# Kernel tuning notes

Hardware: AMD Instinct MI355X
Metric: run time of the kernel (lower is better)

Reference implementation:

```python
import jax, jax.numpy as jnp
import numpy as np

B, T, C, L = 512, 512, 96, 64   # batch, time steps, num classes (incl. blank), max label len
BLANK = C - 1                   # keras ctc_batch_cost uses last class as blank
EPS = 1e-7                      # epsilon added before log, as in ctc_batch_cost
NEG = -1e30                     # log-space -inf surrogate


def setup_inputs():
    key = jax.random.key(0)
    k1, k2, k3 = jax.random.split(key, 3)
    # y_pred is a softmax output: positive, rows sum to 1
    u = jax.random.uniform(k1, (B, T, C), dtype=jnp.float32, minval=0.1, maxval=1.0)
    y_pred = u / jnp.sum(u, axis=-1, keepdims=True)
    # labels in [0, BLANK), variable lengths, padded with -1 (as the layer expects)
    labels = jax.random.randint(k2, (B, L), 0, C - 1, dtype=jnp.int32)
    lens = jax.random.randint(k3, (B,), L // 2, L + 1, dtype=jnp.int32)
    y_true = jnp.where(jnp.arange(L)[None, :] < lens[:, None], labels, -1)
    return {"y_true": y_true, "y_pred": y_pred}


def _ctc_loss(y_true, y_pred):
    """Per-example CTC negative log-likelihood (forward DP in log space)."""
    y_true = y_true.astype(jnp.int32)
    lbl_len = jnp.sum((y_true != -1).astype(jnp.int32), axis=-1)          # (B,)
    labels = jnp.where(y_true != -1, y_true, 0)                            # (B,L)

    S = 2 * L + 1
    # extended label: blank, l0, blank, l1, ..., blank
    ext = jnp.full((B, S), BLANK, dtype=jnp.int32).at[:, 1::2].set(labels)  # (B,S)
    ext_m2 = jnp.pad(ext[:, :-2], ((0, 0), (2, 0)), constant_values=BLANK)
    can_skip = (ext != BLANK) & (ext != ext_m2)                             # (B,S)

    lp = jnp.log(y_pred.astype(jnp.float32) + EPS)   # (B,T,C) log-probs
    lp_t = jnp.swapaxes(lp, 0, 1)                    # (T,B,C) for scan over time

    emit0 = jnp.take_along_axis(lp_t[0], ext, axis=1)                       # (B,S)
    alpha0 = (jnp.full((B, S), NEG, dtype=jnp.float32)
              .at[:, 0].set(emit0[:, 0])
              .at[:, 1].set(emit0[:, 1]))

    def step(alpha, lpt):
        a1 = jnp.pad(alpha[:, :-1], ((0, 0), (1, 0)), constant_values=NEG)
        a2 = jnp.pad(alpha[:, :-2], ((0, 0), (2, 0)), constant_values=NEG)
        a2 = jnp.where(can_skip, a2, NEG)
        m = jnp.maximum(alpha, jnp.maximum(a1, a2))
        lse = m + jnp.log(jnp.exp(alpha - m) + jnp.exp(a1 - m) + jnp.exp(a2 - m))
        alpha_new = lse + jnp.take_along_axis(lpt, ext, axis=1)
        return alpha_new, None

    alphaT, _ = jax.lax.scan(step, alpha0, lp_t[1:])

    # total log-prob ends at last blank (s=2*len) or last label (s=2*len-1)
    i_blank = (2 * lbl_len)[:, None]
    i_label = jnp.maximum(2 * lbl_len - 1, 0)[:, None]
    a_b = jnp.take_along_axis(alphaT, i_blank, axis=1)[:, 0]
    a_l = jnp.take_along_axis(alphaT, i_label, axis=1)[:, 0]
    return -jnp.logaddexp(a_b, a_l)                                         # (B,)


def reference(y_true, y_pred):
    # layer adds tf.reduce_mean(ctc_batch_cost(...)) as the model loss
    return jnp.mean(_ctc_loss(y_true, y_pred))
```

## Files before the change

### kernel.cpp

```cpp
#include <hip/hip_runtime.h>


#define B_ 512
#define T_ 512
#define C_ 96
#define L_ 64
#define BLANK_ 95
#define EPSF 1e-7f
#define LN2F 0.69314718055994530942f

template <int CTRL>
__device__ __forceinline__ float dpp_mov(float x) {
    return __int_as_float(
        __builtin_amdgcn_update_dpp(0, __float_as_int(x), CTRL, 0xF, 0xF, true));
}

__device__ __forceinline__ float wave_max(float m) {
    m = fmaxf(m, dpp_mov<0x111>(m));
    m = fmaxf(m, dpp_mov<0x112>(m));
    m = fmaxf(m, dpp_mov<0x114>(m));
    m = fmaxf(m, dpp_mov<0x118>(m));
    m = fmaxf(m, dpp_mov<0x142>(m));
    m = fmaxf(m, dpp_mov<0x143>(m));
    return __int_as_float(__builtin_amdgcn_readlane(__float_as_int(m), 63));
}

__launch_bounds__(64, 1)
__global__ void ctc_loss_kernel(const int* __restrict__ y_true,
                                const float* __restrict__ y_pred,
                                float* __restrict__ out) {
    const int b = blockIdx.x;
    const int lane = threadIdx.x;

    const int yv = y_true[b * L_ + lane];
    const unsigned long long act = __ballot(yv != -1);
    const int len = __popcll(act);
    const int lab = (yv == -1) ? 0 : yv;
    const int lab_prev = __shfl_up(lab, 1);
    const bool cs = (lane == 0) ? true : (lab != lab_prev);

    const float* rowp = y_pred + (size_t)b * T_ * C_;
    const float* plp = rowp + lab;
    const float* pbp = rowp + BLANK_;

    constexpr int U = 8;
    constexpr int D = 8;
    constexpr int NCH = T_ / U;
    float bl[D][U], bb[D][U];
#pragma unroll
    for (int d = 0; d < D; ++d)
#pragma unroll
        for (int k = 0; k < U; ++k) {
            bl[d][k] = plp[(d * U + k) * C_];
            bb[d][k] = pbp[(d * U + k) * C_];
        }

    float a_even, a_odd, a128;
    int accum = -96;
    a_even = (lane == 0) ? ldexpf(bb[0][0] + EPSF, 96) : 0.0f;
    a_odd  = (lane == 0) ? ldexpf(bl[0][0] + EPSF, 96) : 0.0f;
    a128 = 0.0f;

    auto chunk_exec = [&](const float* cl, const float* cb, int kstart) {
        float pl[U], pb[U], mpl[U];
#pragma unroll
        for (int k = 0; k < U; ++k) {
            pl[k] = cl[k] + EPSF;
            pb[k] = cb[k] + EPSF;
            mpl[k] = cs ? pl[k] : 0.0f;
        }
#pragma unroll
        for (int k = 0; k < U; ++k) {
            if (k < kstart) continue;
            const float po = dpp_mov<0x138>(a_odd);
            const float ne = fmaf(po, pb[k], a_even * pb[k]);
            const float no = fmaf(po, mpl[k], (a_odd + a_even) * pl[k]);
            a128 = fmaf(a_odd, pb[k], a128 * pb[k]);
            a_even = ne;
            a_odd = no;
        }
        const float mv = wave_max(fmaxf(fmaxf(a_even, a_odd), a128));
        const int e = ((__float_as_int(mv) >> 23) & 0xFF) - 126;
        const int kk = 96 - e;
        a_even = ldexpf(a_even, kk);
        a_odd  = ldexpf(a_odd, kk);
        a128   = ldexpf(a128, kk);
        accum -= kk;
    };

    auto prefetch = [&](float* dl, float* db, int t0) {
#pragma unroll
        for (int k = 0; k < U; ++k) {
            dl[k] = plp[(t0 + k) * C_];
            db[k] = pbp[(t0 + k) * C_];
        }
    };

#pragma unroll
    for (int sub = 0; sub < D; ++sub) {
        chunk_exec(bl[sub], bb[sub], (sub == 0) ? 1 : 0);
        prefetch(bl[sub], bb[sub], (sub + D) * U);
    }

    for (int g = 1; g < NCH / D; ++g) {
#pragma unroll
        for (int sub = 0; sub < D; ++sub) {
            const int c = g * D + sub;
            chunk_exec(bl[sub], bb[sub], 0);
            if (c + D < NCH) prefetch(bl[sub], bb[sub], (c + D) * U);
        }
    }

    const float al = __shfl(a_odd, len - 1);
    const float ab = (len < L_) ? __shfl(a_even, len)
                                : __shfl(a128, 63);
    if (lane == 0) {
        const float loss = -LN2F * (log2f(ab + al) + (float)accum);
        atomicAdd(out, loss * (1.0f / B_));
    }
}

extern "C" void kernel_launch(void* const* d_in, const int* in_sizes, int n_in,
                              void* d_out, int out_size, void* d_ws, size_t ws_size,
                              hipStream_t stream) {
    const int* y_true = (const int*)d_in[0];
    const float* y_pred = (const float*)d_in[1];
    float* out = (float*)d_out;
    hipMemsetAsync(out, 0, sizeof(float), stream);
    ctc_loss_kernel<<<B_, 64, 0, stream>>>(y_true, y_pred, out);
}
```

Measured before the change: 156.9 us.

## Stage y_pred chunks through double-buffered LDS with coalesced float4 loads

Each lane used to do scalar strided gathers from global memory for its label column and the blank column at every timestep. Now whole 8-timestep chunks are loaded with coalesced float4 reads into a register ring four chunks deep. They are copied into a double-buffered LDS slot and gathered from there. The t=0 initialisation is folded into the recurrence by seeding lane 0's even state with 2^96, so the first step needs no special case. This cuts global load instruction count and uncoalesced traffic, but puts LDS round-trip latency and extra writes onto the serial DP chain.

After: 192.1 us. 1.22x slower.

```diff
diff --git a/kernel.cpp b/kernel.cpp
--- a/kernel.cpp
+++ b/kernel.cpp
@@ -39,75 +39,78 @@
     const int lab_prev = __shfl_up(lab, 1);
     const bool cs = (lane == 0) ? true : (lab != lab_prev);
 
-    const float* rowp = y_pred + (size_t)b * T_ * C_;
-    const float* plp = rowp + lab;
-    const float* pbp = rowp + BLANK_;
+    constexpr int U = 8;
+    constexpr int D = 4;
+    constexpr int NCH = T_ / U;
+    constexpr int CHW = U * C_;
 
-    constexpr int U = 8;
-    constexpr int D = 8;
-    constexpr int NCH = T_ / U;
-    float bl[D][U], bb[D][U];
+    const float* __restrict__ gbase = y_pred + (size_t)b * T_ * C_ + lane * 4;
+
+    __shared__ __align__(16) float smem[2 * CHW];
+
+    float4 ring[D][3];
 #pragma unroll
     for (int d = 0; d < D; ++d)
 #pragma unroll
-        for (int k = 0; k < U; ++k) {
-            bl[d][k] = plp[(d * U + k) * C_];
-            bb[d][k] = pbp[(d * U + k) * C_];
-        }
+        for (int j = 0; j < 3; ++j)
+            ring[d][j] = *reinterpret_cast<const float4*>(gbase + d * CHW + j * 256);
+#pragma unroll
+    for (int j = 0; j < 3; ++j)
+        *reinterpret_cast<float4*>(&smem[(j * 64 + lane) * 4]) = ring[0][j];
 
-    float a_even, a_odd, a128;
+    float a_even = (lane == 0) ? 0x1.0p96f : 0.0f;
+    float a_odd = 0.0f;
+    float a128 = 0.0f;
     int accum = -96;
-    a_even = (lane == 0) ? ldexpf(bb[0][0] + EPSF, 96) : 0.0f;
-    a_odd  = (lane == 0) ? ldexpf(bl[0][0] + EPSF, 96) : 0.0f;
-    a128 = 0.0f;
 
-    auto chunk_exec = [&](const float* cl, const float* cb, int kstart) {
-        float pl[U], pb[U], mpl[U];
+    for (int cc = 0; cc < NCH; cc += D) {
 #pragma unroll
-        for (int k = 0; k < U; ++k) {
-            pl[k] = cl[k] + EPSF;
-            pb[k] = cb[k] + EPSF;
-            mpl[k] = cs ? pl[k] : 0.0f;
-        }
+        for (int sub = 0; sub < D; ++sub) {
+            const int c = cc + sub;
+
+            if (c + D < NCH) {
 #pragma unroll
-        for (int k = 0; k < U; ++k) {
-            if (k < kstart) continue;
-            const float po = dpp_mov<0x138>(a_odd);
-            const float ne = fmaf(po, pb[k], a_even * pb[k]);
-            const float no = fmaf(po, mpl[k], (a_odd + a_even) * pl[k]);
-            a128 = fmaf(a_odd, pb[k], a128 * pb[k]);
-            a_even = ne;
-            a_odd = no;
-        }
-        const float mv = wave_max(fmaxf(fmaxf(a_even, a_odd), a128));
-        const int e = ((__float_as_int(mv) >> 23) & 0xFF) - 126;
-        const int kk = 96 - e;
-        a_even = ldexpf(a_even, kk);
-        a_odd  = ldexpf(a_odd, kk);
-        a128   = ldexpf(a128, kk);
-        accum -= kk;
-    };
+                for (int j = 0; j < 3; ++j)
+                    ring[sub][j] = *reinterpret_cast<const float4*>(
+                        gbase + (c + D) * CHW + j * 256);
+            }
 
-    auto prefetch = [&](float* dl, float* db, int t0) {
+            constexpr int U_ = U;
+            const int slot = sub & 1;
+            float pl[U_], pb[U_], mpl[U_];
 #pragma unroll
-        for (int k = 0; k < U; ++k) {
-            dl[k] = plp[(t0 + k) * C_];
-            db[k] = pbp[(t0 + k) * C_];
-        }
-    };
+            for (int k = 0; k < U_; ++k) {
+                pl[k] = smem[slot * CHW + k * C_ + lab] + EPSF;
+                pb[k] = smem[slot * CHW + k * C_ + BLANK_] + EPSF;
+                mpl[k] = cs ? pl[k] : 0.0f;
+            }
+
+            if (c + 1 < NCH) {
+                const int nslot = (sub + 1) & 1;
+                const int nr = (sub + 1) % D;
+#pragma unroll
+                for (int j = 0; j < 3; ++j)
+                    *reinterpret_cast<float4*>(
+                        &smem[nslot * CHW + (j * 64 + lane) * 4]) = ring[nr][j];
+            }
 
 #pragma unroll
-    for (int sub = 0; sub < D; ++sub) {
-        chunk_exec(bl[sub], bb[sub], (sub == 0) ? 1 : 0);
-        prefetch(bl[sub], bb[sub], (sub + D) * U);
-    }
+            for (int k = 0; k < U_; ++k) {
+                const float po = dpp_mov<0x138>(a_odd);
+                const float ne = fmaf(po, pb[k], a_even * pb[k]);
+                const float no = fmaf(po, mpl[k], (a_odd + a_even) * pl[k]);
+                a128 = fmaf(a_odd, pb[k], a128 * pb[k]);
+                a_even = ne;
+                a_odd = no;
+            }
 
-    for (int g = 1; g < NCH / D; ++g) {
-#pragma unroll
-        for (int sub = 0; sub < D; ++sub) {
-            const int c = g * D + sub;
-            chunk_exec(bl[sub], bb[sub], 0);
-            if (c + D < NCH) prefetch(bl[sub], bb[sub], (c + D) * U);
+            const float mv = wave_max(fmaxf(fmaxf(a_even, a_odd), a128));
+            const int e = ((__float_as_int(mv) >> 23) & 0xFF) - 126;
+            const int kk = 96 - e;
+            a_even = ldexpf(a_even, kk);
+            a_odd = ldexpf(a_odd, kk);
+            a128 = ldexpf(a128, kk);
+            accum -= kk;
         }
     }
 
```
